# Optimization experiments

Hardware: AMD Instinct MI355X
Metric: run time of the kernel (lower is better)

## Reference

```python
import jax, jax.numpy as jnp
import numpy as np

N, C, P, K = 100000, 64, 64, 16  # points, in_planes, planes, nsample
EPS = 1e-5

def _bn(y, g, b, m, v):
    # inference-mode batchnorm over channel (last) dim
    return (y - m) * (g * jax.lax.rsqrt(v + EPS)) + b

def setup_inputs() -> dict:
    key = jax.random.key(0)
    ks = jax.random.split(key, 12)
    p = jax.random.normal(ks[0], (N, 3), jnp.float32)
    x = jax.random.normal(ks[1], (N, C), jnp.float32)
    idx = jax.random.randint(ks[2], (N, K), 0, N, jnp.int32)
    s = 0.05
    w1 = jax.random.normal(ks[3], (C, P), jnp.float32) * s
    conv_w = jax.random.normal(ks[4], (P, P + 3), jnp.float32) * s  # Conv1d(P+3, P, 1) weight squeezed
    w3 = jax.random.normal(ks[5], (P, P), jnp.float32) * s
    def bn_params(k):
        k1, k2 = jax.random.split(k)
        return (jnp.ones((P,), jnp.float32),                      # gamma
                jnp.zeros((P,), jnp.float32),                     # beta
                jax.random.normal(k1, (P,), jnp.float32) * 0.01,  # running mean
                jnp.abs(jax.random.normal(k2, (P,), jnp.float32)) * 0.1 + 1.0)  # running var
    g1, b1, m1, v1 = bn_params(ks[6])
    g2, b2, m2, v2 = bn_params(ks[7])
    g3, b3, m3, v3 = bn_params(ks[8])
    return dict(p=p, x=x, idx=idx, w1=w1, g1=g1, b1=b1, m1=m1, v1=v1,
                conv_w=conv_w, g2=g2, b2=b2, m2=m2, v2=v2,
                w3=w3, g3=g3, b3=b3, m3=m3, v3=v3)

def reference(p, x, idx, w1, g1, b1, m1, v1, conv_w, g2, b2, m2, v2, w3, g3, b3, m3, v3):
    identity = x
    h = jax.nn.relu(_bn(x @ w1, g1, b1, m1, v1))                     # [N, P]
    # queryandgroup with use_xyz=True: concat(relative xyz, neighbor feats)
    rel = p[idx] - p[:, None, :]                                      # [N, K, 3]
    grouped = jnp.concatenate([rel, h[idx]], axis=-1)                 # [N, K, 3+P]
    e = jnp.einsum('nkc,oc->nko', grouped, conv_w)                    # conv1x1 -> [N, K, P]
    e = jax.nn.relu(_bn(e, g2, b2, m2, v2))
    f = jnp.max(e, axis=1)                                            # max over neighbors -> [N, P]
    out = jax.nn.relu(_bn(f @ w3, g3, b3, m3, v3) + identity)         # [N, P]
    return out
```

## Files before the change

kernel.cpp:

```cpp
#include <hip/hip_runtime.h>
#include <stdint.h>


#define EPS 1e-5f

typedef unsigned short u16;
typedef unsigned int u32;
typedef __attribute__((ext_vector_type(8))) short bf16x8;
typedef __attribute__((ext_vector_type(4))) float f32x4;

__device__ __forceinline__ float b2f(u16 u) { return __uint_as_float(((u32)u) << 16); }
__device__ __forceinline__ u16 f2b(float f) {
    u32 u = __float_as_uint(f);
    u32 r = u + 0x7fffu + ((u >> 16) & 1u);
    return (u16)(r >> 16);
}
__device__ __forceinline__ bool is_bf16(const void* g) { return ((const u32*)g)[0] == 0x3F803F80u; }
__device__ __forceinline__ float ldval(const void* p, size_t i, bool isbf) {
    return isbf ? b2f(((const u16*)p)[i]) : ((const float*)p)[i];
}
#define MFMA16(a, b, c) __builtin_amdgcn_mfma_f32_16x16x32_bf16(a, b, c, 0, 0, 0)

__device__ __forceinline__ bf16x8 asbf(uint4 u) {
    union { uint4 u; bf16x8 b; } c;
    c.u = u;
    return c.b;
}

__device__ __forceinline__ bf16x8 ldrow8(const void* base, size_t row, int coff, bool isbf) {
    if (isbf) {
        const u16* pp = (const u16*)base + row * 64 + coff;
        return asbf(*(const uint4*)pp);
    } else {
        const float* pp = (const float*)base + row * 64 + coff;
        float4 q0 = ((const float4*)pp)[0], q1 = ((const float4*)pp)[1];
        bf16x8 r;
        r[0] = (short)f2b(q0.x); r[1] = (short)f2b(q0.y);
        r[2] = (short)f2b(q0.z); r[3] = (short)f2b(q0.w);
        r[4] = (short)f2b(q1.x); r[5] = (short)f2b(q1.y);
        r[6] = (short)f2b(q1.z); r[7] = (short)f2b(q1.w);
        return r;
    }
}

__global__ void __launch_bounds__(256)
k_prep(const void* __restrict__ w1, const void* __restrict__ cw, const void* __restrict__ w3,
       const void* __restrict__ g1, const void* __restrict__ b1, const void* __restrict__ m1,
       const void* __restrict__ v1, const void* __restrict__ g2, const void* __restrict__ b2,
       const void* __restrict__ m2, const void* __restrict__ v2, const void* __restrict__ g3,
       const void* __restrict__ b3, const void* __restrict__ m3, const void* __restrict__ v3,
       uint4* __restrict__ w1f, uint4* __restrict__ cwf, uint4* __restrict__ w3f,
       float* __restrict__ bnst) {
    const bool isbf = is_bf16(g1);
    const int tid = blockIdx.x * blockDim.x + threadIdx.x;
    if (tid < 512) {
        int f = tid >> 6, lane = tid & 63;
        int ch = f >> 2, t = f & 3, quad = lane >> 4, c0 = lane & 15;
        union { uint4 u; bf16x8 b; } r;
#pragma unroll
        for (int j = 0; j < 8; ++j) {
            int c = ch * 32 + quad * 8 + j, o = t * 16 + c0;
            r.b[j] = (short)f2b(ldval(w1, (size_t)c * 64 + o, isbf));
        }
        w1f[f * 64 + lane] = r.u;
    } else if (tid < 1280) {
        int f = (tid - 512) >> 6, lane = tid & 63;
        int ch = f >> 2, t = f & 3, quad = lane >> 4, c0 = lane & 15;
        union { uint4 u; bf16x8 b; } r;
#pragma unroll
        for (int j = 0; j < 8; ++j) {
            int o = t * 16 + c0;
            short val;
            if (ch < 2) {
                int c = ch * 32 + quad * 8 + j;
                val = (short)f2b(ldval(cw, (size_t)o * 67 + 3 + c, isbf));
            } else {
                int pc = quad * 8 + j;
                val = (pc < 3) ? (short)f2b(ldval(cw, (size_t)o * 67 + pc, isbf)) : (short)0;
            }
            r.b[j] = val;
        }
        cwf[f * 64 + lane] = r.u;
    } else if (tid < 1792) {
        int f = (tid - 1280) >> 6, lane = tid & 63;
        int ch = f >> 2, t = f & 3, quad = lane >> 4, c0 = lane & 15;
        union { uint4 u; bf16x8 b; } r;
#pragma unroll
        for (int j = 0; j < 8; ++j) {
            int c = ch * 32 + quad * 8 + j, o = t * 16 + c0;
            r.b[j] = (short)f2b(ldval(w3, (size_t)c * 64 + o, isbf));
        }
        w3f[f * 64 + lane] = r.u;
    } else if (tid < 2176) {
        int id = tid - 1792;
        int bn = id >> 7, rem = id & 127, ch = rem & 63, which = rem >> 6;
        const void* g = (bn == 0) ? g1 : (bn == 1) ? g2 : g3;
        const void* b = (bn == 0) ? b1 : (bn == 1) ? b2 : b3;
        const void* m = (bn == 0) ? m1 : (bn == 1) ? m2 : m3;
        const void* v = (bn == 0) ? v1 : (bn == 1) ? v2 : v3;
        float gv = ldval(g, ch, isbf), bv = ldval(b, ch, isbf);
        float mv = ldval(m, ch, isbf), vv = ldval(v, ch, isbf);
        float s = gv * rsqrtf(vv + EPS);
        float t = bv - mv * s;
        bnst[bn * 128 + which * 64 + ch] = which ? t : s;
    }
}

__global__ void __launch_bounds__(256, 4)
k_h_mfma(const void* __restrict__ x, const void* __restrict__ p, const void* __restrict__ g1,
         const uint4* __restrict__ w1f, const float* __restrict__ bnst,
         float4* __restrict__ p4, u16* __restrict__ hbf, int N) {
    const bool isbf = is_bf16(g1);
    const int lane = threadIdx.x & 63, quad = lane >> 4, col = lane & 15;
    const int wave = blockIdx.x * (blockDim.x >> 6) + (threadIdx.x >> 6);
    const int nw = gridDim.x * (blockDim.x >> 6);
    bf16x8 B00 = asbf(w1f[0 * 64 + lane]), B01 = asbf(w1f[1 * 64 + lane]);
    bf16x8 B02 = asbf(w1f[2 * 64 + lane]), B03 = asbf(w1f[3 * 64 + lane]);
    bf16x8 B10 = asbf(w1f[4 * 64 + lane]), B11 = asbf(w1f[5 * 64 + lane]);
    bf16x8 B12 = asbf(w1f[6 * 64 + lane]), B13 = asbf(w1f[7 * 64 + lane]);
    f32x4 sv, tv;
#pragma unroll
    for (int t = 0; t < 4; ++t) {
        sv[t] = bnst[0 * 128 + 0 + t * 16 + col];
        tv[t] = bnst[0 * 128 + 64 + t * 16 + col];
    }
    const int nt = (N + 15) >> 4;
    for (int ti = wave; ti < nt; ti += nw) {
        const int n0 = ti * 16;
        int ra = n0 + col;
        if (ra > N - 1) ra = N - 1;
        bf16x8 A0 = ldrow8(x, (size_t)ra, quad * 8, isbf);
        bf16x8 A1 = ldrow8(x, (size_t)ra, 32 + quad * 8, isbf);
        if (quad == 0 && n0 + col < N) {
            int row = n0 + col;
            float4 pv;
            pv.x = ldval(p, (size_t)row * 3 + 0, isbf);
            pv.y = ldval(p, (size_t)row * 3 + 1, isbf);
            pv.z = ldval(p, (size_t)row * 3 + 2, isbf);
            pv.w = 0.f;
            p4[row] = pv;
        }
        f32x4 acc0 = {0.f, 0.f, 0.f, 0.f}, acc1 = acc0, acc2 = acc0, acc3 = acc0;
        acc0 = MFMA16(A0, B00, acc0); acc0 = MFMA16(A1, B10, acc0);
        acc1 = MFMA16(A0, B01, acc1); acc1 = MFMA16(A1, B11, acc1);
        acc2 = MFMA16(A0, B02, acc2); acc2 = MFMA16(A1, B12, acc2);
        acc3 = MFMA16(A0, B03, acc3); acc3 = MFMA16(A1, B13, acc3);
#define STT(acc, t)                                                            \
    {                                                                          \
        _Pragma("unroll") for (int r = 0; r < 4; ++r) {                        \
            int row = n0 + quad * 4 + r;                                       \
            if (row < N) {                                                     \
                float e = acc[r] * sv[t] + tv[t];                              \
                hbf[(size_t)row * 64 + (t)*16 + col] = f2b(fmaxf(e, 0.f));     \
            }                                                                  \
        }                                                                      \
    }
        STT(acc0, 0) STT(acc1, 1) STT(acc2, 2) STT(acc3, 3)
#undef STT
    }
}

template <bool FORCE_BF16>
__global__ void __launch_bounds__(256, 3)
k_conv_mfma(const u16* __restrict__ hbf, const float4* __restrict__ p4,
            const int* __restrict__ idx, const uint4* __restrict__ cwf,
            const float* __restrict__ bnst, const void* __restrict__ g2,
            void* __restrict__ fout, int N) {
    const bool isbf = is_bf16(g2);
    const int lane = threadIdx.x & 63, quad = lane >> 4, col = lane & 15;
    const int wave = blockIdx.x * (blockDim.x >> 6) + (threadIdx.x >> 6);
    const int nw = gridDim.x * (blockDim.x >> 6);
    bf16x8 B00 = asbf(cwf[0 * 64 + lane]), B01 = asbf(cwf[1 * 64 + lane]);
    bf16x8 B02 = asbf(cwf[2 * 64 + lane]), B03 = asbf(cwf[3 * 64 + lane]);
    bf16x8 B10 = asbf(cwf[4 * 64 + lane]), B11 = asbf(cwf[5 * 64 + lane]);
    bf16x8 B12 = asbf(cwf[6 * 64 + lane]), B13 = asbf(cwf[7 * 64 + lane]);
    bf16x8 B20 = asbf(cwf[8 * 64 + lane]), B21 = asbf(cwf[9 * 64 + lane]);
    bf16x8 B22 = asbf(cwf[10 * 64 + lane]), B23 = asbf(cwf[11 * 64 + lane]);
    f32x4 sv, tv;
#pragma unroll
    for (int t = 0; t < 4; ++t) {
        sv[t] = bnst[1 * 128 + 0 + t * 16 + col];
        tv[t] = bnst[1 * 128 + 64 + t * 16 + col];
    }
    const int step = 2 * nw;
    int b = 2 * wave;
    int ja_c = 0, jb_c = 0;
    uint4 h0a_c, h1a_c, h0b_c, h1b_c;
    if (b < N) {
        const int na = b, nb = (b + 1 < N) ? b + 1 : b;
        ja_c = idx[(size_t)na * 16 + col];
        jb_c = idx[(size_t)nb * 16 + col];
        const uint4* ra = (const uint4*)(hbf + (size_t)ja_c * 64);
        const uint4* rb = (const uint4*)(hbf + (size_t)jb_c * 64);
        h0a_c = ra[quad]; h1a_c = ra[4 + quad];
        h0b_c = rb[quad]; h1b_c = rb[4 + quad];
    }
    for (; b < N; b += step) {
        const int bnext = b + step;
        int ja_n = 0, jb_n = 0;
        uint4 h0a_n = {0, 0, 0, 0}, h1a_n = h0a_n, h0b_n = h0a_n, h1b_n = h0a_n;
        if (bnext < N) {
            const int na = bnext, nb = (bnext + 1 < N) ? bnext + 1 : bnext;
            ja_n = idx[(size_t)na * 16 + col];
            jb_n = idx[(size_t)nb * 16 + col];
            const uint4* ra = (const uint4*)(hbf + (size_t)ja_n * 64);
            const uint4* rb = (const uint4*)(hbf + (size_t)jb_n * 64);
            h0a_n = ra[quad]; h1a_n = ra[4 + quad];
            h0b_n = rb[quad]; h1b_n = rb[4 + quad];
        }
        const int na = b, nb = (b + 1 < N) ? b + 1 : b;
        float4 pja = p4[ja_c], pjb = p4[jb_c];
        float4 pna = p4[na], pnb = p4[nb];
        bf16x8 A2a = {0, 0, 0, 0, 0, 0, 0, 0}, A2b = A2a;
        if (quad == 0) {
            A2a[0] = (short)f2b(pja.x - pna.x);
            A2a[1] = (short)f2b(pja.y - pna.y);
            A2a[2] = (short)f2b(pja.z - pna.z);
            A2b[0] = (short)f2b(pjb.x - pnb.x);
            A2b[1] = (short)f2b(pjb.y - pnb.y);
            A2b[2] = (short)f2b(pjb.z - pnb.z);
        }
        f32x4 z = {0.f, 0.f, 0.f, 0.f};
        f32x4 acc0a = z, acc1a = z, acc2a = z, acc3a = z;
        f32x4 acc0b = z, acc1b = z, acc2b = z, acc3b = z;
        bf16x8 a0a = asbf(h0a_c), a1a = asbf(h1a_c);
        bf16x8 a0b = asbf(h0b_c), a1b = asbf(h1b_c);
        acc0a = MFMA16(a0a, B00, acc0a); acc0b = MFMA16(a0b, B00, acc0b);
        acc1a = MFMA16(a0a, B01, acc1a); acc1b = MFMA16(a0b, B01, acc1b);
        acc2a = MFMA16(a0a, B02, acc2a); acc2b = MFMA16(a0b, B02, acc2b);
        acc3a = MFMA16(a0a, B03, acc3a); acc3b = MFMA16(a0b, B03, acc3b);
        acc0a = MFMA16(a1a, B10, acc0a); acc0b = MFMA16(a1b, B10, acc0b);
        acc1a = MFMA16(a1a, B11, acc1a); acc1b = MFMA16(a1b, B11, acc1b);
        acc2a = MFMA16(a1a, B12, acc2a); acc2b = MFMA16(a1b, B12, acc2b);
        acc3a = MFMA16(a1a, B13, acc3a); acc3b = MFMA16(a1b, B13, acc3b);
        acc0a = MFMA16(A2a, B20, acc0a); acc0b = MFMA16(A2b, B20, acc0b);
        acc1a = MFMA16(A2a, B21, acc1a); acc1b = MFMA16(A2b, B21, acc1b);
        acc2a = MFMA16(A2a, B22, acc2a); acc2b = MFMA16(A2b, B22, acc2b);
        acc3a = MFMA16(A2a, B23, acc3a); acc3b = MFMA16(A2b, B23, acc3b);
#define RED(acc, t, dst)                                                       \
    {                                                                          \
        float mx = fmaxf(fmaxf(acc[0], acc[1]), fmaxf(acc[2], acc[3]));        \
        float mn = fminf(fminf(acc[0], acc[1]), fminf(acc[2], acc[3]));        \
        mx = fmaxf(mx, __shfl_xor(mx, 16));                                    \
        mn = fminf(mn, __shfl_xor(mn, 16));                                    \
        mx = fmaxf(mx, __shfl_xor(mx, 32));                                    \
        mn = fminf(mn, __shfl_xor(mn, 32));                                    \
        float e = fmaxf(sv[t] * mx + tv[t], sv[t] * mn + tv[t]);               \
        dst = fmaxf(e, 0.f);                                                   \
    }
        {
            float f0, f1, f2, f3;
            RED(acc0a, 0, f0) RED(acc1a, 1, f1) RED(acc2a, 2, f2) RED(acc3a, 3, f3)
            float fv = (lane < 16) ? f0 : (lane < 32) ? f1 : (lane < 48) ? f2 : f3;
            if (FORCE_BF16 || isbf)
                ((u16*)fout)[(size_t)na * 64 + lane] = f2b(fv);
            else
                ((float*)fout)[(size_t)na * 64 + lane] = fv;
        }
        if (b + 1 < N) {
            float f0, f1, f2, f3;
            RED(acc0b, 0, f0) RED(acc1b, 1, f1) RED(acc2b, 2, f2) RED(acc3b, 3, f3)
            float fv = (lane < 16) ? f0 : (lane < 32) ? f1 : (lane < 48) ? f2 : f3;
            if (FORCE_BF16 || isbf)
                ((u16*)fout)[(size_t)nb * 64 + lane] = f2b(fv);
            else
                ((float*)fout)[(size_t)nb * 64 + lane] = fv;
        }
#undef RED
        ja_c = ja_n; jb_c = jb_n;
        h0a_c = h0a_n; h1a_c = h1a_n; h0b_c = h0b_n; h1b_c = h1b_n;
    }
}

template <bool FIN_BF16_ALWAYS>
__global__ void __launch_bounds__(256, 4)
k_out_mfma(const void* __restrict__ fin, const void* __restrict__ x,
           const uint4* __restrict__ w3f, const float* __restrict__ bnst,
           const void* __restrict__ g3, void* __restrict__ out, int N) {
    const bool isbf = is_bf16(g3);
    const bool finbf = FIN_BF16_ALWAYS ? true : isbf;
    const int lane = threadIdx.x & 63, quad = lane >> 4, col = lane & 15;
    const int wave = blockIdx.x * (blockDim.x >> 6) + (threadIdx.x >> 6);
    const int nw = gridDim.x * (blockDim.x >> 6);
    bf16x8 B00 = asbf(w3f[0 * 64 + lane]), B01 = asbf(w3f[1 * 64 + lane]);
    bf16x8 B02 = asbf(w3f[2 * 64 + lane]), B03 = asbf(w3f[3 * 64 + lane]);
    bf16x8 B10 = asbf(w3f[4 * 64 + lane]), B11 = asbf(w3f[5 * 64 + lane]);
    bf16x8 B12 = asbf(w3f[6 * 64 + lane]), B13 = asbf(w3f[7 * 64 + lane]);
    f32x4 sv, tv;
#pragma unroll
    for (int t = 0; t < 4; ++t) {
        sv[t] = bnst[2 * 128 + 0 + t * 16 + col];
        tv[t] = bnst[2 * 128 + 64 + t * 16 + col];
    }
    const int nt = (N + 15) >> 4;
    for (int ti = wave; ti < nt; ti += nw) {
        const int n0 = ti * 16;
        int ra = n0 + col;
        if (ra > N - 1) ra = N - 1;
        bf16x8 A0 = ldrow8(fin, (size_t)ra, quad * 8, finbf);
        bf16x8 A1 = ldrow8(fin, (size_t)ra, 32 + quad * 8, finbf);
        f32x4 acc0 = {0.f, 0.f, 0.f, 0.f}, acc1 = acc0, acc2 = acc0, acc3 = acc0;
        acc0 = MFMA16(A0, B00, acc0); acc0 = MFMA16(A1, B10, acc0);
        acc1 = MFMA16(A0, B01, acc1); acc1 = MFMA16(A1, B11, acc1);
        acc2 = MFMA16(A0, B02, acc2); acc2 = MFMA16(A1, B12, acc2);
        acc3 = MFMA16(A0, B03, acc3); acc3 = MFMA16(A1, B13, acc3);
#define STT(acc, t)                                                            \
    {                                                                          \
        _Pragma("unroll") for (int r = 0; r < 4; ++r) {                        \
            int row = n0 + quad * 4 + r;                                       \
            if (row < N) {                                                     \
                int o_ = (t)*16 + col;                                         \
                float e = acc[r] * sv[t] + tv[t] +                             \
                          ldval(x, (size_t)row * 64 + o_, isbf);               \
                e = fmaxf(e, 0.f);                                             \
                if (isbf)                                                      \
                    ((u16*)out)[(size_t)row * 64 + o_] = f2b(e);               \
                else                                                           \
                    ((float*)out)[(size_t)row * 64 + o_] = e;                  \
            }                                                                  \
        }                                                                      \
    }
        STT(acc0, 0) STT(acc1, 1) STT(acc2, 2) STT(acc3, 3)
#undef STT
    }
}

__device__ __forceinline__ void load_col64(const void* w, int lane, bool isbf, float* col) {
#pragma unroll
    for (int c = 0; c < 64; ++c) col[c] = ldval(w, (size_t)c * 64 + lane, isbf);
}
__device__ __forceinline__ float dot64(const void* x, size_t off, bool isbf, const float* col) {
    float a0 = 0.f;
#pragma unroll
    for (int c = 0; c < 64; ++c) a0 += ldval(x, off + c, isbf) * col[c];
    return a0;
}
__device__ __forceinline__ void bn_st(const void* g, const void* b, const void* m,
                                      const void* v, int o, bool isbf, float& s, float& t) {
    float gv = ldval(g, o, isbf), bv = ldval(b, o, isbf);
    float mv = ldval(m, o, isbf), vv = ldval(v, o, isbf);
    s = gv * rsqrtf(vv + EPS);
    t = bv - mv * s;
}
__global__ void __launch_bounds__(256) k_mono(const void* __restrict__ p, const void* __restrict__ x,
                                              const int* __restrict__ idx, const void* __restrict__ w1,
                                              const void* __restrict__ g1, const void* __restrict__ b1,
                                              const void* __restrict__ m1, const void* __restrict__ v1,
                                              const void* __restrict__ cw, const void* __restrict__ g2,
                                              const void* __restrict__ b2, const void* __restrict__ m2,
                                              const void* __restrict__ v2, const void* __restrict__ w3,
                                              const void* __restrict__ g3, const void* __restrict__ b3,
                                              const void* __restrict__ m3, const void* __restrict__ v3,
                                              void* __restrict__ out, int N) {
    const bool isbf = is_bf16(g1);
    const int lane = threadIdx.x & 63;
    const int wave = blockIdx.x * (blockDim.x >> 6) + (threadIdx.x >> 6);
    const int nw = gridDim.x * (blockDim.x >> 6);
    float w1col[64];
    load_col64(w1, lane, isbf, w1col);
    float w3col[64];
    load_col64(w3, lane, isbf, w3col);
    float s1, t1, s2, t2, s3, t3;
    bn_st(g1, b1, m1, v1, lane, isbf, s1, t1);
    bn_st(g2, b2, m2, v2, lane, isbf, s2, t2);
    bn_st(g3, b3, m3, v3, lane, isbf, s3, t3);
    for (int n = wave; n < N; n += nw) {
        const int4* ir = (const int4*)(idx + (size_t)n * 16);
        float pnx = ldval(p, (size_t)n * 3 + 0, isbf);
        float pny = ldval(p, (size_t)n * 3 + 1, isbf);
        float pnz = ldval(p, (size_t)n * 3 + 2, isbf);
        float fmx = 0.f;
        for (int kk = 0; kk < 4; ++kk) {
            const int4 iv = ir[kk];
#pragma unroll
            for (int t = 0; t < 4; ++t) {
                const int j = (t == 0) ? iv.x : (t == 1) ? iv.y : (t == 2) ? iv.z : iv.w;
                float hr = dot64(x, (size_t)j * 64, isbf, w1col);
                float hv = fmaxf(hr * s1 + t1, 0.f);
                float a0 = (ldval(p, (size_t)j * 3 + 0, isbf) - pnx) * ldval(cw, (size_t)lane * 67 + 0, isbf) +
                           (ldval(p, (size_t)j * 3 + 1, isbf) - pny) * ldval(cw, (size_t)lane * 67 + 1, isbf) +
                           (ldval(p, (size_t)j * 3 + 2, isbf) - pnz) * ldval(cw, (size_t)lane * 67 + 2, isbf);
#pragma unroll
                for (int c = 0; c < 64; ++c)
                    a0 += __shfl(hv, c) * ldval(cw, (size_t)lane * 67 + 3 + c, isbf);
                fmx = fmaxf(fmx, a0 * s2 + t2);
            }
        }
        float a = 0.f;
#pragma unroll
        for (int c = 0; c < 64; ++c) a += __shfl(fmx, c) * w3col[c];
        float r = a * s3 + t3 + ldval(x, (size_t)n * 64 + lane, isbf);
        r = fmaxf(r, 0.f);
        if (isbf)
            ((u16*)out)[(size_t)n * 64 + lane] = f2b(r);
        else
            ((float*)out)[(size_t)n * 64 + lane] = r;
    }
}

extern "C" void kernel_launch(void* const* d_in, const int* in_sizes, int n_in,
                              void* d_out, int out_size, void* d_ws, size_t ws_size,
                              hipStream_t stream) {
    const void* p = d_in[0];
    const void* x = d_in[1];
    const int* idx = (const int*)d_in[2];
    const void* w1 = d_in[3];
    const void* g1 = d_in[4];
    const void* b1 = d_in[5];
    const void* m1 = d_in[6];
    const void* v1 = d_in[7];
    const void* cw = d_in[8];
    const void* g2 = d_in[9];
    const void* b2 = d_in[10];
    const void* m2 = d_in[11];
    const void* v2 = d_in[12];
    const void* w3 = d_in[13];
    const void* g3 = d_in[14];
    const void* b3 = d_in[15];
    const void* m3 = d_in[16];
    const void* v3 = d_in[17];
    const int N = in_sizes[0] / 3;

    const int blk = 256;
    const int nt = (N + 15) >> 4;
    const int gh = (nt + 3) >> 2;
    const int gc = 768;

    const size_t hb = (size_t)N * 64 * sizeof(u16);
    const size_t p4b = (size_t)N * sizeof(float4);
    const size_t packb = 8192 + 12288 + 8192 + 1536;
    const size_t need_hf = 256 + 2 * hb + p4b + packb;
    const size_t need_h = 256 + hb + p4b + packb;

    if (ws_size >= need_h) {
        char* base = (char*)d_ws + 256;
        const bool big = (ws_size >= need_hf);
        u16* h = (u16*)base;
        u16* f = big ? (u16*)(base + hb) : nullptr;
        char* rest = base + (big ? 2 * hb : hb);
        float4* p4 = (float4*)rest;
        uint4* w1f = (uint4*)(rest + p4b);
        uint4* cwf = (uint4*)(rest + p4b + 8192);
        uint4* w3f = (uint4*)(rest + p4b + 8192 + 12288);
        float* bnst = (float*)(rest + p4b + 8192 + 12288 + 8192);
        k_prep<<<9, blk, 0, stream>>>(w1, cw, w3, g1, b1, m1, v1, g2, b2, m2, v2,
                                      g3, b3, m3, v3, w1f, cwf, w3f, bnst);
        k_h_mfma<<<gh, blk, 0, stream>>>(x, p, g1, w1f, bnst, p4, h, N);
        if (big) {
            k_conv_mfma<true><<<gc, blk, 0, stream>>>(h, p4, idx, cwf, bnst, g2, (void*)f, N);
            k_out_mfma<true><<<gh, blk, 0, stream>>>((const void*)f, x, w3f, bnst, g3, d_out, N);
        } else {
            k_conv_mfma<false><<<gc, blk, 0, stream>>>(h, p4, idx, cwf, bnst, g2, d_out, N);
            k_out_mfma<false><<<gh, blk, 0, stream>>>((const void*)d_out, x, w3f, bnst, g3, d_out, N);
        }
    } else {
        k_mono<<<2048, blk, 0, stream>>>(p, x, idx, w1, g1, b1, m1, v1, cw, g2, b2, m2, v2,
                                         w3, g3, b3, m3, v3, d_out, N);
    }
}
```

Measured before the change: 179.5 us.

## Deepen gather prefetch pipeline in conv kernel and raise occupancy and grid

The conv kernel now prefetches neighbour indices two iterations ahead and neighbour features plus neighbour positions one iteration ahead. This removes the dependent idx→hbf load chain and the p4 gather from the critical path of each step. Launch bounds move from 3 to 4 waves-per-EU and the grid grows from 768 to 1792 blocks, giving more memory-level parallelism for the random gathers. The extra prefetch registers may conflict with the tighter register budget under the higher occupancy target and could cause spills.

```diff
diff --git a/kernel.cpp b/kernel.cpp
--- a/kernel.cpp
+++ b/kernel.cpp
@@ -161,7 +161,7 @@
 }
 
 template <bool FORCE_BF16>
-__global__ void __launch_bounds__(256, 3)
+__global__ void __launch_bounds__(256, 4)
 k_conv_mfma(const u16* __restrict__ hbf, const float4* __restrict__ p4,
             const int* __restrict__ idx, const uint4* __restrict__ cwf,
             const float* __restrict__ bnst, const void* __restrict__ g2,
@@ -184,47 +184,52 @@
     }
     const int step = 2 * nw;
     int b = 2 * wave;
-    int ja_c = 0, jb_c = 0;
-    uint4 h0a_c, h1a_c, h0b_c, h1b_c;
-    if (b < N) {
+    if (b >= N) return;
+    int ja = idx[(size_t)b * 16 + col];
+    int jb = idx[(size_t)((b + 1 < N) ? b + 1 : b) * 16 + col];
+    const uint4* ra0 = (const uint4*)(hbf + (size_t)ja * 64);
+    const uint4* rb0 = (const uint4*)(hbf + (size_t)jb * 64);
+    uint4 h0aC = ra0[quad], h1aC = ra0[4 + quad];
+    uint4 h0bC = rb0[quad], h1bC = rb0[4 + quad];
+    float4 pjaC = p4[ja], pjbC = p4[jb];
+    int jaN, jbN;
+    {
+        int bn1 = b + step;
+        int na = (bn1 < N) ? bn1 : b;
+        int nb = (bn1 + 1 < N) ? bn1 + 1 : na;
+        jaN = idx[(size_t)na * 16 + col];
+        jbN = idx[(size_t)nb * 16 + col];
+    }
+    for (; b < N; b += step) {
+        int jaN2, jbN2;
+        {
+            int b2 = b + 2 * step;
+            int na = (b2 < N) ? b2 : b;
+            int nb = (b2 + 1 < N) ? b2 + 1 : na;
+            jaN2 = idx[(size_t)na * 16 + col];
+            jbN2 = idx[(size_t)nb * 16 + col];
+        }
+        const uint4* ra = (const uint4*)(hbf + (size_t)jaN * 64);
+        const uint4* rb = (const uint4*)(hbf + (size_t)jbN * 64);
+        uint4 h0aN = ra[quad], h1aN = ra[4 + quad];
+        uint4 h0bN = rb[quad], h1bN = rb[4 + quad];
+        float4 pjaN = p4[jaN], pjbN = p4[jbN];
         const int na = b, nb = (b + 1 < N) ? b + 1 : b;
-        ja_c = idx[(size_t)na * 16 + col];
-        jb_c = idx[(size_t)nb * 16 + col];
-        const uint4* ra = (const uint4*)(hbf + (size_t)ja_c * 64);
-        const uint4* rb = (const uint4*)(hbf + (size_t)jb_c * 64);
-        h0a_c = ra[quad]; h1a_c = ra[4 + quad];
-        h0b_c = rb[quad]; h1b_c = rb[4 + quad];
-    }
-    for (; b < N; b += step) {
-        const int bnext = b + step;
-        int ja_n = 0, jb_n = 0;
-        uint4 h0a_n = {0, 0, 0, 0}, h1a_n = h0a_n, h0b_n = h0a_n, h1b_n = h0a_n;
-        if (bnext < N) {
-            const int na = bnext, nb = (bnext + 1 < N) ? bnext + 1 : bnext;
-            ja_n = idx[(size_t)na * 16 + col];
-            jb_n = idx[(size_t)nb * 16 + col];
-            const uint4* ra = (const uint4*)(hbf + (size_t)ja_n * 64);
-            const uint4* rb = (const uint4*)(hbf + (size_t)jb_n * 64);
-            h0a_n = ra[quad]; h1a_n = ra[4 + quad];
-            h0b_n = rb[quad]; h1b_n = rb[4 + quad];
-        }
-        const int na = b, nb = (b + 1 < N) ? b + 1 : b;
-        float4 pja = p4[ja_c], pjb = p4[jb_c];
         float4 pna = p4[na], pnb = p4[nb];
         bf16x8 A2a = {0, 0, 0, 0, 0, 0, 0, 0}, A2b = A2a;
         if (quad == 0) {
-            A2a[0] = (short)f2b(pja.x - pna.x);
-            A2a[1] = (short)f2b(pja.y - pna.y);
-            A2a[2] = (short)f2b(pja.z - pna.z);
-            A2b[0] = (short)f2b(pjb.x - pnb.x);
-            A2b[1] = (short)f2b(pjb.y - pnb.y);
-            A2b[2] = (short)f2b(pjb.z - pnb.z);
+            A2a[0] = (short)f2b(pjaC.x - pna.x);
+            A2a[1] = (short)f2b(pjaC.y - pna.y);
+            A2a[2] = (short)f2b(pjaC.z - pna.z);
+            A2b[0] = (short)f2b(pjbC.x - pnb.x);
+            A2b[1] = (short)f2b(pjbC.y - pnb.y);
+            A2b[2] = (short)f2b(pjbC.z - pnb.z);
         }
         f32x4 z = {0.f, 0.f, 0.f, 0.f};
         f32x4 acc0a = z, acc1a = z, acc2a = z, acc3a = z;
         f32x4 acc0b = z, acc1b = z, acc2b = z, acc3b = z;
-        bf16x8 a0a = asbf(h0a_c), a1a = asbf(h1a_c);
-        bf16x8 a0b = asbf(h0b_c), a1b = asbf(h1b_c);
+        bf16x8 a0a = asbf(h0aC), a1a = asbf(h1aC);
+        bf16x8 a0b = asbf(h0bC), a1b = asbf(h1bC);
         acc0a = MFMA16(a0a, B00, acc0a); acc0b = MFMA16(a0b, B00, acc0b);
         acc1a = MFMA16(a0a, B01, acc1a); acc1b = MFMA16(a0b, B01, acc1b);
         acc2a = MFMA16(a0a, B02, acc2a); acc2b = MFMA16(a0b, B02, acc2b);
@@ -267,8 +272,9 @@
                 ((float*)fout)[(size_t)nb * 64 + lane] = fv;
         }
 #undef RED
-        ja_c = ja_n; jb_c = jb_n;
-        h0a_c = h0a_n; h1a_c = h1a_n; h0b_c = h0b_n; h1b_c = h1b_n;
+        h0aC = h0aN; h1aC = h1aN; h0bC = h0bN; h1bC = h1bN;
+        pjaC = pjaN; pjbC = pjbN;
+        jaN = jaN2; jbN = jbN2;
     }
 }
 
@@ -424,7 +430,7 @@
     const int blk = 256;
     const int nt = (N + 15) >> 4;
     const int gh = (nt + 3) >> 2;
-    const int gc = 768;
+    const int gc = 1792;
 
     const size_t hb = (size_t)N * 64 * sizeof(u16);
     const size_t p4b = (size_t)N * sizeof(float4);
```

New measurement: 219.6 us. 22.4% more time.
